# Performance work log

Measured on AMD Instinct MI355X. Metric: run time of the kernel, lower is better.

## Reference

```python
import jax, jax.numpy as jnp
import numpy as np

DIM = 1024
HEADS = 16
EPS = 1e-05
B, T, C, H, W = 2, 16, DIM, 32, 32


def setup_inputs() -> dict:
    key = jax.random.key(0)
    ks = jax.random.split(key, 4)
    s = 1.0 / np.sqrt(DIM)
    return {
        "x": jax.random.normal(ks[0], (B, T, C, H, W), dtype=jnp.float32),
        "ln_w": jnp.ones((C,), dtype=jnp.float32),
        "ln_b": jnp.zeros((C,), dtype=jnp.float32),
        "Wq": jax.random.normal(ks[1], (C, C), dtype=jnp.float32) * s,
        "Wk": jax.random.normal(ks[2], (C, C), dtype=jnp.float32) * s,
        "Wv": jax.random.normal(ks[3], (C, C), dtype=jnp.float32) * s,
    }


def reference(x, ln_w, ln_b, Wq, Wk, Wv):
    b, t, c, h, w = x.shape
    heads = HEADS
    dh = c // heads
    scale = dh ** (-0.5)

    # Channel LayerNorm: normalize over C per (b,t,h,w)
    xc = jnp.transpose(x, (0, 1, 3, 4, 2))  # [B,T,H,W,C]
    mu = jnp.mean(xc, axis=-1, keepdims=True)
    var = jnp.mean(jnp.square(xc - mu), axis=-1, keepdims=True)
    xn = (xc - mu) * jax.lax.rsqrt(var + EPS) * ln_w + ln_b  # [B,T,H,W,C]

    # Q/K from spatial mean-pool
    pooled = jnp.mean(xn, axis=(2, 3))  # [B,T,C]
    q = pooled @ Wq.T  # [B,T,C]
    k = pooled @ Wk.T  # [B,T,C]

    # V per pixel; torch permutes to [B,W,H,T,C] then flattens W-major
    v = jnp.transpose(xn, (0, 3, 2, 1, 4)).reshape(b, h * w, t, c)  # [B,HW(w-major),T,C]
    v = v @ Wv.T

    q = q.reshape(b, t, heads, dh).transpose(0, 2, 1, 3) * scale  # [B,h,T,dh]
    k = k.reshape(b, t, heads, dh).transpose(0, 2, 3, 1)          # [B,h,dh,T]
    v = v.reshape(b, h * w, t, heads, dh).transpose(0, 1, 3, 2, 4)  # [B,HW,h,T,dh]

    attn = jax.nn.softmax(jnp.matmul(q, k), axis=-1)  # [B,h,T,T]
    out = jnp.einsum('bhst,bnhtd->bnhsd', attn, v)    # [B,HW,h,T,dh]
    # permute(0,3,2,4,1) -> [B,T,h,dh,HW], then view as (H,W)
    out = out.transpose(0, 3, 2, 4, 1).reshape(b, t, c, h, w)
    return out
```

## Files before the change

### kernel.cpp

```cpp
#include <hip/hip_runtime.h>
#include <stdint.h>
#include <stddef.h>

#define CDIM 1024
#define HWD  1024
#define TD   16
#define BD   2
#define NH   16
#define DHD  64

typedef __attribute__((ext_vector_type(8))) short bf16x8;
typedef __attribute__((ext_vector_type(4))) short bf16x4;
typedef __attribute__((ext_vector_type(4))) float f32x4;

static __device__ __forceinline__ short f2bf(float f) {
  uint32_t u = __builtin_bit_cast(uint32_t, f);
  uint32_t r = (u + 0x7FFFu + ((u >> 16) & 1u)) >> 16;
  return (short)(uint16_t)r;
}
static __device__ __forceinline__ float bf2f(short s) {
  return __builtin_bit_cast(float, (uint32_t)((uint16_t)s) << 16);
}

static __device__ __forceinline__ void gl_lds16(const short* g, short* l) {
  __builtin_amdgcn_global_load_lds((const __attribute__((address_space(1))) unsigned int*)g,
                                   (__attribute__((address_space(3))) unsigned int*)l,
                                   16, 0, 0);
}

__global__ void k_cast_w(const float* __restrict__ W, short* __restrict__ Wb) {
  int i = (blockIdx.x * 256 + threadIdx.x) * 4;
  f32x4 v = *(const f32x4*)&W[i];
  Wb[i + 0] = f2bf(v[0]);
  Wb[i + 1] = f2bf(v[1]);
  Wb[i + 2] = f2bf(v[2]);
  Wb[i + 3] = f2bf(v[3]);
}

__global__ void k_ln_t(const float* __restrict__ x, const float* __restrict__ lnw,
                       const float* __restrict__ lnb, short* __restrict__ xnT) {
  int bt = blockIdx.y;
  int p0 = blockIdx.x * 64;
  int tid = threadIdx.x;
  int pl = tid & 63;
  int cq = tid >> 6;
  const float* xs = x + (size_t)bt * CDIM * HWD;

  float s = 0.f, s2 = 0.f;
  for (int c = cq * 256; c < cq * 256 + 256; ++c) {
    float v = xs[(size_t)c * HWD + p0 + pl];
    s += v; s2 += v * v;
  }
  __shared__ float red[8][64];
  red[cq][pl] = s;
  red[4 + cq][pl] = s2;
  __syncthreads();
  float st  = red[0][pl] + red[1][pl] + red[2][pl] + red[3][pl];
  float st2 = red[4][pl] + red[5][pl] + red[6][pl] + red[7][pl];
  float mu   = st * (1.0f / CDIM);
  float var  = st2 * (1.0f / CDIM) - mu * mu;
  float rstd = rsqrtf(var + 1e-5f);

  __shared__ short tile[64 * 68];
  short* outB = xnT + (size_t)bt * CDIM * HWD;

  for (int cb = 0; cb < 16; ++cb) {
    #pragma unroll
    for (int cc2 = 0; cc2 < 16; ++cc2) {
      int c = cb * 64 + cq * 16 + cc2;
      float v = xs[(size_t)c * HWD + p0 + pl];
      float xn = (v - mu) * rstd * lnw[c] + lnb[c];
      tile[pl * 68 + cq * 16 + cc2] = f2bf(xn);
    }
    __syncthreads();
    #pragma unroll
    for (int it = 0; it < 2; ++it) {
      int ch = it * 256 + tid;
      int plo = ch >> 3;
      int c8 = (ch & 7) * 8;
      bf16x4 a = *(const bf16x4*)&tile[plo * 68 + c8];
      bf16x4 b = *(const bf16x4*)&tile[plo * 68 + c8 + 4];
      int pq = p0 + plo;
      int q = (pq & 31) * 32 + (pq >> 5);
      short* dst = outB + (size_t)q * CDIM + cb * 64 + c8;
      *(bf16x4*)dst = a;
      *(bf16x4*)(dst + 4) = b;
    }
    __syncthreads();
  }
}

__global__ void k_pool_part(const short* __restrict__ xnT, float* __restrict__ part) {
  int bt = blockIdx.y, pc = blockIdx.x;
  int c8 = threadIdx.x * 8;
  const short* base = xnT + (size_t)bt * CDIM * HWD;
  float s[8] = {};
  for (int p = pc * 128; p < pc * 128 + 128; ++p) {
    bf16x8 v = *(const bf16x8*)&base[(size_t)p * CDIM + c8];
    #pragma unroll
    for (int k = 0; k < 8; ++k) s[k] += bf2f(v[k]);
  }
  float* pr = part + ((size_t)pc * BD * TD + bt) * CDIM + c8;
  #pragma unroll
  for (int k = 0; k < 8; ++k) pr[k] = s[k];
}
__global__ void k_pool_red(const float* __restrict__ part, float* __restrict__ pooled,
                           short* __restrict__ pooledb) {
  int bt = blockIdx.y;
  int c = blockIdx.x * 256 + threadIdx.x;
  float s = 0.f;
  #pragma unroll
  for (int pc = 0; pc < 8; ++pc) s += part[((size_t)pc * BD * TD + bt) * CDIM + c];
  float m = s * (1.0f / HWD);
  pooled[bt * CDIM + c] = m;
  pooledb[bt * CDIM + c] = f2bf(m);
}

__global__ __launch_bounds__(256) void k_qk_mfma(const short* __restrict__ Wqkb,
                                                 const short* __restrict__ pooledb,
                                                 float* __restrict__ qm,
                                                 float* __restrict__ km) {
  int n0 = blockIdx.x * 128;
  __shared__ __align__(16) short lA[32 * 32];
  __shared__ __align__(16) short lB[128 * 32];
  int tid = threadIdx.x, lane = tid & 63, wid = tid >> 6;
  int s0 = wid * 128 + lane, s1 = s0 + 64;
  int fr = lane & 15, fk = (lane >> 4) * 8;
  f32x4 acc[2][2] = {};

  for (int kt = 0; kt < CDIM / 32; ++kt) {
    int k0 = kt * 32;
    __syncthreads();
    gl_lds16(&Wqkb[(size_t)(n0 + (s0 >> 2)) * CDIM + k0 + (s0 & 3) * 8], &lB[s0 * 8]);
    gl_lds16(&Wqkb[(size_t)(n0 + (s1 >> 2)) * CDIM + k0 + (s1 & 3) * 8], &lB[s1 * 8]);
    if (wid < 2) {
      gl_lds16(&pooledb[(size_t)(tid >> 2) * CDIM + k0 + (tid & 3) * 8], &lA[tid * 8]);
    }
    __syncthreads();
    bf16x8 af[2], bfr[2];
    #pragma unroll
    for (int mi = 0; mi < 2; ++mi)
      af[mi] = *(const bf16x8*)&lA[(mi * 16 + fr) * 32 + fk];
    #pragma unroll
    for (int ni = 0; ni < 2; ++ni)
      bfr[ni] = *(const bf16x8*)&lB[(wid * 32 + ni * 16 + fr) * 32 + fk];
    #pragma unroll
    for (int mi = 0; mi < 2; ++mi)
      #pragma unroll
      for (int ni = 0; ni < 2; ++ni)
        acc[mi][ni] = __builtin_amdgcn_mfma_f32_16x16x32_bf16(af[mi], bfr[ni], acc[mi][ni], 0, 0, 0);
  }

  int cr = lane >> 4;
  #pragma unroll
  for (int mi = 0; mi < 2; ++mi)
    #pragma unroll
    for (int ni = 0; ni < 2; ++ni)
      #pragma unroll
      for (int rr = 0; rr < 4; ++rr) {
        int row = mi * 16 + cr * 4 + rr;
        int col = n0 + wid * 32 + ni * 16 + fr;
        float v = acc[mi][ni][rr];
        if (col < 1024) qm[(size_t)row * CDIM + col] = v;
        else            km[(size_t)row * CDIM + col - 1024] = v;
      }
}

__global__ void k_attn(const float* __restrict__ qm, const float* __restrict__ km,
                       float* __restrict__ attn) {
  int bg = blockIdx.x;
  int b = bg >> 4, g = bg & 15;
  int s = threadIdx.x >> 4, t = threadIdx.x & 15;
  const float* qr = qm + (size_t)(b * TD + s) * CDIM + g * DHD;
  const float* kr = km + (size_t)(b * TD + t) * CDIM + g * DHD;
  float d = 0.f;
  #pragma unroll
  for (int i = 0; i < DHD; ++i) d += qr[i] * kr[i];
  d *= 0.125f;
  float m = d;
  #pragma unroll
  for (int off = 8; off; off >>= 1) m = fmaxf(m, __shfl_xor(m, off, 16));
  float e = __expf(d - m);
  float sum = e;
  #pragma unroll
  for (int off = 8; off; off >>= 1) sum += __shfl_xor(sum, off, 16);
  attn[(size_t)bg * 256 + s * 16 + t] = e / sum;
}

__global__ __launch_bounds__(512, 2) void k_vgemm(const short* __restrict__ Wb,
                                                  const short* __restrict__ xnT,
                                                  short* __restrict__ vp) {
  int bid = blockIdx.x;
  int swz = (bid & 7) * 64 + (bid >> 3);
  int bt = swz >> 4;
  int m0 = ((swz >> 2) & 3) * 256;
  int n0 = (swz & 3) * 256;
  const short* Bm = xnT + (size_t)bt * CDIM * HWD;

  __shared__ __align__(16) short lA[2][256 * 64];
  __shared__ __align__(16) short lB[2][256 * 64];

  int tid = threadIdx.x, lane = tid & 63, wid = tid >> 6;
  int wm = wid >> 2, wn = wid & 3;

  int srow = wid * 8 + (lane >> 3);
  int schunk = (lane & 7) ^ (lane >> 3);
  const short* gA = Wb + (size_t)(m0 + srow) * CDIM + schunk * 8;
  const short* gB = Bm + (size_t)(n0 + srow) * CDIM + schunk * 8;
  int doff = wid * 512 + lane * 8;

  int fr = lane & 15, klane = lane >> 4;
  int c0 = ((klane ^ (fr & 7)) * 8);
  int rA = (wm * 128 + fr) * 64;
  int rB = (wn * 64 + fr) * 64;

  f32x4 acc[8][4] = {};
  bf16x8 bq[4], af[4];

#define ISSUE(p, kt1, nb)                                                      \
  do {                                                                         \
    gl_lds16(gA + (size_t)(p) * 64 * CDIM + (kt1) * 64, &lA[nb][(p) * 4096 + doff]); \
    gl_lds16(gB + (size_t)(p) * 64 * CDIM + (kt1) * 64, &lB[nb][(p) * 4096 + doff]); \
  } while (0)
#define RDA(mi, ks, b) (*(const bf16x8*)&lA[b][rA + (mi) * 1024 + (c0 ^ ((ks) * 32))])
#define RDB(ni, ks, b) (*(const bf16x8*)&lB[b][rB + (ni) * 1024 + (c0 ^ ((ks) * 32))])

  ISSUE(0, 0, 0); ISSUE(1, 0, 0); ISSUE(2, 0, 0); ISSUE(3, 0, 0);

  for (int kt = 0; kt < 16; ++kt) {
    int cur = kt & 1, nxt = cur ^ 1;
    bool st = (kt + 1 < 16);
    if (st) {
      ISSUE(0, kt + 1, nxt);
      asm volatile("s_waitcnt vmcnt(2)" ::: "memory");
    } else {
      asm volatile("s_waitcnt vmcnt(0)" ::: "memory");
    }
    __builtin_amdgcn_s_barrier();
    #pragma unroll
    for (int ni = 0; ni < 4; ++ni) bq[ni] = RDB(ni, 0, cur);
    #pragma unroll
    for (int mi = 0; mi < 4; ++mi) af[mi] = RDA(mi, 0, cur);
    __builtin_amdgcn_s_setprio(1);
    #pragma unroll
    for (int mi = 0; mi < 4; ++mi)
      #pragma unroll
      for (int ni = 0; ni < 4; ++ni)
        acc[mi][ni] = __builtin_amdgcn_mfma_f32_16x16x32_bf16(af[mi], bq[ni], acc[mi][ni], 0, 0, 0);
    __builtin_amdgcn_s_setprio(0);
    __builtin_amdgcn_s_barrier();
    #pragma unroll
    for (int mi = 0; mi < 4; ++mi) af[mi] = RDA(4 + mi, 0, cur);
    if (st) ISSUE(1, kt + 1, nxt);
    __builtin_amdgcn_s_barrier();
    __builtin_amdgcn_s_setprio(1);
    #pragma unroll
    for (int mi = 0; mi < 4; ++mi)
      #pragma unroll
      for (int ni = 0; ni < 4; ++ni)
        acc[4 + mi][ni] = __builtin_amdgcn_mfma_f32_16x16x32_bf16(af[mi], bq[ni], acc[4 + mi][ni], 0, 0, 0);
    __builtin_amdgcn_s_setprio(0);
    __builtin_amdgcn_s_barrier();
    #pragma unroll
    for (int ni = 0; ni < 4; ++ni) bq[ni] = RDB(ni, 1, cur);
    #pragma unroll
    for (int mi = 0; mi < 4; ++mi) af[mi] = RDA(mi, 1, cur);
    if (st) ISSUE(2, kt + 1, nxt);
    __builtin_amdgcn_s_barrier();
    __builtin_amdgcn_s_setprio(1);
    #pragma unroll
    for (int mi = 0; mi < 4; ++mi)
      #pragma unroll
      for (int ni = 0; ni < 4; ++ni)
        acc[mi][ni] = __builtin_amdgcn_mfma_f32_16x16x32_bf16(af[mi], bq[ni], acc[mi][ni], 0, 0, 0);
    __builtin_amdgcn_s_setprio(0);
    __builtin_amdgcn_s_barrier();
    #pragma unroll
    for (int mi = 0; mi < 4; ++mi) af[mi] = RDA(4 + mi, 1, cur);
    if (st) ISSUE(3, kt + 1, nxt);
    __builtin_amdgcn_s_barrier();
    __builtin_amdgcn_s_setprio(1);
    #pragma unroll
    for (int mi = 0; mi < 4; ++mi)
      #pragma unroll
      for (int ni = 0; ni < 4; ++ni)
        acc[4 + mi][ni] = __builtin_amdgcn_mfma_f32_16x16x32_bf16(af[mi], bq[ni], acc[4 + mi][ni], 0, 0, 0);
    __builtin_amdgcn_s_setprio(0);
    __builtin_amdgcn_s_barrier();
  }
#undef ISSUE
#undef RDA
#undef RDB

  short* outB = vp + (size_t)bt * CDIM * HWD;
  int cr = lane >> 4;
  #pragma unroll
  for (int mi = 0; mi < 8; ++mi)
    #pragma unroll
    for (int ni = 0; ni < 4; ++ni)
      #pragma unroll
      for (int r = 0; r < 4; ++r) {
        int row = m0 + wm * 128 + mi * 16 + cr * 4 + r;
        int col = n0 + wn * 64 + ni * 16 + fr;
        outB[(size_t)row * HWD + col] = f2bf(acc[mi][ni][r]);
      }
}

__global__ __launch_bounds__(256) void k_mix(const short* __restrict__ vp,
                                             const float* __restrict__ attn,
                                             float* __restrict__ out) {
  int c = blockIdx.x;
  int b = blockIdx.y;
  int g = c >> 6;
  __shared__ __align__(16) short vpl[TD * HWD];
  __shared__ float at[256];
  int tid = threadIdx.x;
  at[tid] = attn[(size_t)(b * NH + g) * 256 + tid];
  #pragma unroll
  for (int j = 0; j < 8; ++j) {
    int chunk = j * 256 + tid;
    int t = chunk >> 7, qc = chunk & 127;
    bf16x8 v = *(const bf16x8*)&vp[((size_t)(b * TD + t) * CDIM + c) * HWD + qc * 8];
    *(bf16x8*)&vpl[t * HWD + qc * 8] = v;
  }
  __syncthreads();
  int p = tid * 4;
  #pragma unroll
  for (int sh = 0; sh < 2; ++sh) {
    f32x4 acc[8] = {};
    #pragma unroll
    for (int t = 0; t < TD; ++t) {
      bf16x4 v4 = *(const bf16x4*)&vpl[t * HWD + p];
      f32x4 vf = {bf2f(v4[0]), bf2f(v4[1]), bf2f(v4[2]), bf2f(v4[3])};
      #pragma unroll
      for (int s8 = 0; s8 < 8; ++s8) {
        float a = at[(sh * 8 + s8) * 16 + t];
        acc[s8] += a * vf;
      }
    }
    #pragma unroll
    for (int s8 = 0; s8 < 8; ++s8) {
      int s = sh * 8 + s8;
      *(f32x4*)&out[((size_t)(b * TD + s) * CDIM + c) * HWD + p] = acc[s8];
    }
  }
}

extern "C" void kernel_launch(void* const* d_in, const int* in_sizes, int n_in,
                              void* d_out, int out_size, void* d_ws, size_t ws_size,
                              hipStream_t stream) {
  const float* x   = (const float*)d_in[0];
  const float* lnw = (const float*)d_in[1];
  const float* lnb = (const float*)d_in[2];
  const float* Wq  = (const float*)d_in[3];
  const float* Wk  = (const float*)d_in[4];
  const float* Wv  = (const float*)d_in[5];
  float* out = (float*)d_out;

  char* ws = (char*)d_ws;
  const size_t XNT_OFF   = 0;
  const size_t VP_OFF    = XNT_OFF + 67108864;
  const size_t WB_OFF    = VP_OFF + 67108864;
  const size_t WQKB_OFF  = WB_OFF + 2097152;
  const size_t POOLP_OFF = WQKB_OFF + 4194304;
  const size_t POOL_OFF  = POOLP_OFF + 1048576;
  const size_t POOLB_OFF = POOL_OFF + 131072;
  const size_t QM_OFF    = POOLB_OFF + 65536;
  const size_t KM_OFF    = QM_OFF + 131072;
  const size_t ATTN_OFF  = KM_OFF + 131072;

  short* xnT    = (short*)(ws + XNT_OFF);
  short* vp     = (short*)(ws + VP_OFF);
  short* Wb     = (short*)(ws + WB_OFF);
  short* Wqkb   = (short*)(ws + WQKB_OFF);
  float* poolp  = (float*)(ws + POOLP_OFF);
  float* pooled = (float*)(ws + POOL_OFF);
  short* poolb  = (short*)(ws + POOLB_OFF);
  float* qm     = (float*)(ws + QM_OFF);
  float* km     = (float*)(ws + KM_OFF);
  float* attn   = (float*)(ws + ATTN_OFF);

  k_cast_w<<<dim3(1024), 256, 0, stream>>>(Wv, Wb);
  k_cast_w<<<dim3(1024), 256, 0, stream>>>(Wq, Wqkb);
  k_cast_w<<<dim3(1024), 256, 0, stream>>>(Wk, Wqkb + 1048576);
  k_ln_t<<<dim3(16, 32), 256, 0, stream>>>(x, lnw, lnb, xnT);
  k_pool_part<<<dim3(8, 32), 128, 0, stream>>>(xnT, poolp);
  k_pool_red<<<dim3(4, 32), 256, 0, stream>>>(poolp, pooled, poolb);
  k_qk_mfma<<<dim3(16), 256, 0, stream>>>(Wqkb, poolb, qm, km);
  k_attn<<<dim3(32), 256, 0, stream>>>(qm, km, attn);
  k_vgemm<<<dim3(512), 512, 0, stream>>>(Wb, xnT, vp);
  k_mix<<<dim3(1024, 2), 256, 0, stream>>>(vp, attn, out);
}
```

Baseline: 226.6 us.

## Fuse spatial pooling into LayerNorm, vectorize LN loads, batch vgemm prefetch issues

Partial spatial sums are now computed inside the LayerNorm/transpose kernel, which removes the separate pooling kernel that re-read the whole bf16 xnT tensor. The LN kernel also switches to float4 loads with 4 pixels per thread and a 16-way channel split for the statistics pass. In the V GEMM, all four prefetch groups for the next k-tile are issued at the top of the iteration rather than spread between MFMA phases. The pooled mean is now summed from fp32 normalized values instead of bf16-rounded ones, and the partial buffer grows to 16 slices.

Result: slower. 231.4 us (+2.1%).

```diff
diff --git a/kernel.cpp b/kernel.cpp
--- a/kernel.cpp
+++ b/kernel.cpp
@@ -37,40 +37,67 @@
   Wb[i + 3] = f2bf(v[3]);
 }
 
-__global__ void k_ln_t(const float* __restrict__ x, const float* __restrict__ lnw,
-                       const float* __restrict__ lnb, short* __restrict__ xnT) {
+__global__ __launch_bounds__(256) void k_ln_t(const float* __restrict__ x,
+                                              const float* __restrict__ lnw,
+                                              const float* __restrict__ lnb,
+                                              short* __restrict__ xnT,
+                                              float* __restrict__ part) {
   int bt = blockIdx.y;
   int p0 = blockIdx.x * 64;
   int tid = threadIdx.x;
-  int pl = tid & 63;
-  int cq = tid >> 6;
+  int pg = tid & 15, cs = tid >> 4;
+  int pbase = p0 + pg * 4;
   const float* xs = x + (size_t)bt * CDIM * HWD;
 
-  float s = 0.f, s2 = 0.f;
-  for (int c = cq * 256; c < cq * 256 + 256; ++c) {
-    float v = xs[(size_t)c * HWD + p0 + pl];
-    s += v; s2 += v * v;
-  }
-  __shared__ float red[8][64];
-  red[cq][pl] = s;
-  red[4 + cq][pl] = s2;
+  float s[4] = {}, s2[4] = {};
+  #pragma unroll 8
+  for (int j = 0; j < 64; ++j) {
+    int c = cs + 16 * j;
+    f32x4 v = *(const f32x4*)&xs[(size_t)c * HWD + pbase];
+    #pragma unroll
+    for (int i = 0; i < 4; ++i) { s[i] += v[i]; s2[i] += v[i] * v[i]; }
+  }
+  __shared__ float redA[16][64], redB[16][64];
+  #pragma unroll
+  for (int i = 0; i < 4; ++i) {
+    redA[cs][pg * 4 + i] = s[i];
+    redB[cs][pg * 4 + i] = s2[i];
+  }
   __syncthreads();
-  float st  = red[0][pl] + red[1][pl] + red[2][pl] + red[3][pl];
-  float st2 = red[4][pl] + red[5][pl] + red[6][pl] + red[7][pl];
-  float mu   = st * (1.0f / CDIM);
-  float var  = st2 * (1.0f / CDIM) - mu * mu;
-  float rstd = rsqrtf(var + 1e-5f);
+  __shared__ float muS[64], rsS[64];
+  if (tid < 64) {
+    float a = 0.f, b2 = 0.f;
+    #pragma unroll
+    for (int k = 0; k < 16; ++k) { a += redA[k][tid]; b2 += redB[k][tid]; }
+    float mu = a * (1.0f / CDIM);
+    float var = b2 * (1.0f / CDIM) - mu * mu;
+    muS[tid] = mu;
+    rsS[tid] = rsqrtf(var + 1e-5f);
+  }
+  __syncthreads();
+  float mu_[4], rs_[4];
+  #pragma unroll
+  for (int i = 0; i < 4; ++i) { mu_[i] = muS[pg * 4 + i]; rs_[i] = rsS[pg * 4 + i]; }
 
   __shared__ short tile[64 * 68];
+  __shared__ float pr[64][17];
   short* outB = xnT + (size_t)bt * CDIM * HWD;
 
   for (int cb = 0; cb < 16; ++cb) {
     #pragma unroll
-    for (int cc2 = 0; cc2 < 16; ++cc2) {
-      int c = cb * 64 + cq * 16 + cc2;
-      float v = xs[(size_t)c * HWD + p0 + pl];
-      float xn = (v - mu) * rstd * lnw[c] + lnb[c];
-      tile[pl * 68 + cq * 16 + cc2] = f2bf(xn);
+    for (int jj = 0; jj < 4; ++jj) {
+      int cl = cs * 4 + jj;
+      int c = cb * 64 + cl;
+      f32x4 v = *(const f32x4*)&xs[(size_t)c * HWD + pbase];
+      float w = lnw[c], bb = lnb[c];
+      float psum = 0.f;
+      #pragma unroll
+      for (int i = 0; i < 4; ++i) {
+        float xn = (v[i] - mu_[i]) * rs_[i] * w + bb;
+        tile[(pg * 4 + i) * 68 + cl] = f2bf(xn);
+        psum += xn;
+      }
+      pr[cl][pg] = psum;
     }
     __syncthreads();
     #pragma unroll
@@ -86,31 +113,23 @@
       *(bf16x4*)dst = a;
       *(bf16x4*)(dst + 4) = b;
     }
+    if (tid < 64) {
+      float a = 0.f;
+      #pragma unroll
+      for (int k = 0; k < 16; ++k) a += pr[tid][k];
+      part[((size_t)bt * 16 + blockIdx.x) * CDIM + cb * 64 + tid] = a;
+    }
     __syncthreads();
   }
 }
 
-__global__ void k_pool_part(const short* __restrict__ xnT, float* __restrict__ part) {
-  int bt = blockIdx.y, pc = blockIdx.x;
-  int c8 = threadIdx.x * 8;
-  const short* base = xnT + (size_t)bt * CDIM * HWD;
-  float s[8] = {};
-  for (int p = pc * 128; p < pc * 128 + 128; ++p) {
-    bf16x8 v = *(const bf16x8*)&base[(size_t)p * CDIM + c8];
-    #pragma unroll
-    for (int k = 0; k < 8; ++k) s[k] += bf2f(v[k]);
-  }
-  float* pr = part + ((size_t)pc * BD * TD + bt) * CDIM + c8;
-  #pragma unroll
-  for (int k = 0; k < 8; ++k) pr[k] = s[k];
-}
 __global__ void k_pool_red(const float* __restrict__ part, float* __restrict__ pooled,
                            short* __restrict__ pooledb) {
   int bt = blockIdx.y;
   int c = blockIdx.x * 256 + threadIdx.x;
   float s = 0.f;
   #pragma unroll
-  for (int pc = 0; pc < 8; ++pc) s += part[((size_t)pc * BD * TD + bt) * CDIM + c];
+  for (int pc = 0; pc < 16; ++pc) s += part[((size_t)bt * 16 + pc) * CDIM + c];
   float m = s * (1.0f / HWD);
   pooled[bt * CDIM + c] = m;
   pooledb[bt * CDIM + c] = f2bf(m);
@@ -229,10 +248,10 @@
 
   for (int kt = 0; kt < 16; ++kt) {
     int cur = kt & 1, nxt = cur ^ 1;
-    bool st = (kt + 1 < 16);
-    if (st) {
-      ISSUE(0, kt + 1, nxt);
-      asm volatile("s_waitcnt vmcnt(2)" ::: "memory");
+    if (kt + 1 < 16) {
+      ISSUE(0, kt + 1, nxt); ISSUE(1, kt + 1, nxt);
+      ISSUE(2, kt + 1, nxt); ISSUE(3, kt + 1, nxt);
+      asm volatile("s_waitcnt vmcnt(8)" ::: "memory");
     } else {
       asm volatile("s_waitcnt vmcnt(0)" ::: "memory");
     }
@@ -251,7 +270,6 @@
     __builtin_amdgcn_s_barrier();
     #pragma unroll
     for (int mi = 0; mi < 4; ++mi) af[mi] = RDA(4 + mi, 0, cur);
-    if (st) ISSUE(1, kt + 1, nxt);
     __builtin_amdgcn_s_barrier();
     __builtin_amdgcn_s_setprio(1);
     #pragma unroll
@@ -265,7 +283,6 @@
     for (int ni = 0; ni < 4; ++ni) bq[ni] = RDB(ni, 1, cur);
     #pragma unroll
     for (int mi = 0; mi < 4; ++mi) af[mi] = RDA(mi, 1, cur);
-    if (st) ISSUE(2, kt + 1, nxt);
     __builtin_amdgcn_s_barrier();
     __builtin_amdgcn_s_setprio(1);
     #pragma unroll
@@ -277,7 +294,6 @@
     __builtin_amdgcn_s_barrier();
     #pragma unroll
     for (int mi = 0; mi < 4; ++mi) af[mi] = RDA(4 + mi, 1, cur);
-    if (st) ISSUE(3, kt + 1, nxt);
     __builtin_amdgcn_s_barrier();
     __builtin_amdgcn_s_setprio(1);
     #pragma unroll
@@ -363,7 +379,7 @@
   const size_t WB_OFF    = VP_OFF + 67108864;
   const size_t WQKB_OFF  = WB_OFF + 2097152;
   const size_t POOLP_OFF = WQKB_OFF + 4194304;
-  const size_t POOL_OFF  = POOLP_OFF + 1048576;
+  const size_t POOL_OFF  = POOLP_OFF + 2097152;
   const size_t POOLB_OFF = POOL_OFF + 131072;
   const size_t QM_OFF    = POOLB_OFF + 65536;
   const size_t KM_OFF    = QM_OFF + 131072;
@@ -383,8 +399,7 @@
   k_cast_w<<<dim3(1024), 256, 0, stream>>>(Wv, Wb);
   k_cast_w<<<dim3(1024), 256, 0, stream>>>(Wq, Wqkb);
   k_cast_w<<<dim3(1024), 256, 0, stream>>>(Wk, Wqkb + 1048576);
-  k_ln_t<<<dim3(16, 32), 256, 0, stream>>>(x, lnw, lnb, xnT);
-  k_pool_part<<<dim3(8, 32), 128, 0, stream>>>(xnT, poolp);
+  k_ln_t<<<dim3(16, 32), 256, 0, stream>>>(x, lnw, lnb, xnT, poolp);
   k_pool_red<<<dim3(4, 32), 256, 0, stream>>>(poolp, pooled, poolb);
   k_qk_mfma<<<dim3(16), 256, 0, stream>>>(Wqkb, poolb, qm, km);
   k_attn<<<dim3(32), 256, 0, stream>>>(qm, km, attn);
```
